# Kernel tuning notes

Measured on AMD Instinct MI355X. Metric: run time of the kernel, lower is better.

The kernel has to match this reference:

```python
import jax, jax.numpy as jnp
import numpy as np

BASE_T = 0.07
ALPHA = 0.5
EPS = 1e-12  # torch F.normalize eps


def _l2_normalize(x):
    norm = jnp.linalg.norm(x, axis=1, keepdims=True)
    return x / jnp.maximum(norm, EPS)


def setup_inputs() -> dict:
    key = jax.random.key(0)
    k1, k2, k3 = jax.random.split(key, 3)
    B, D, H, W = 4096, 512, 16, 16
    return {
        "emb1": jax.random.normal(k1, (B, D), dtype=jnp.float32),
        "emb2": jax.random.normal(k2, (B, D), dtype=jnp.float32),
        "attention_map": jax.random.uniform(k3, (B, H, W), dtype=jnp.float32),
    }


def reference(emb1, emb2, attention_map):
    B = emb1.shape[0]
    e1 = _l2_normalize(emb1)
    e2 = _l2_normalize(emb2)

    att = attention_map.mean(axis=(1, 2))                     # [B]
    temp = (BASE_T * (1.0 + ALPHA * att))[:, None]            # [B, 1]

    x = jnp.concatenate([e1, e2], axis=0)                     # [2B, D]
    x_swap = jnp.concatenate([e2, e1], axis=0)                # [2B, D]
    temp_cat = jnp.concatenate([temp, temp], axis=0)          # [2B, 1]

    sim = jnp.matmul(x, x.T) / temp_cat                       # [2B, 2B]
    pos_sim = jnp.sum(x * x_swap, axis=1) / temp_cat[:, 0]    # [2B]

    diag = jnp.eye(2 * B, dtype=bool)
    sim = jnp.where(diag, -jnp.inf, sim)                      # exp(-inf) = 0

    denominator = jnp.exp(sim).sum(axis=1)                    # [2B]
    loss = -jnp.log(jnp.exp(pos_sim) / denominator)
    return loss.mean()
```

## Files before the change

### kernel.cpp

```cpp
#include <hip/hip_runtime.h>
#include <hip/hip_bf16.h>
#include <math.h>

#define B_ROWS 4096
#define D_DIM 512
#define TWO_B 8192
#define HW_N 256
#define BASE_T 0.07f
#define ALPHA_C 0.5f
#define LOG2E 1.44269504088896340736f

typedef float v4f __attribute__((ext_vector_type(4)));

__device__ __forceinline__ float fast_exp2(float x) {
#if __has_builtin(__builtin_amdgcn_exp2f)
    return __builtin_amdgcn_exp2f(x);
#else
    return exp2f(x);
#endif
}

__global__ __launch_bounds__(256) void prep_kernel(
    const float* __restrict__ emb1, const float* __restrict__ emb2,
    const float* __restrict__ att, unsigned short* __restrict__ X8,
    float* __restrict__ inv_temp, float* __restrict__ pos)
{
    const int b = blockIdx.x;
    const int t = threadIdx.x;
    const float2 a1 = ((const float2*)(emb1 + (size_t)b * D_DIM))[t];
    const float2 a2 = ((const float2*)(emb2 + (size_t)b * D_DIM))[t];
    float av = att[(size_t)b * HW_N + t];
    float s1  = a1.x * a1.x + a1.y * a1.y;
    float s2  = a2.x * a2.x + a2.y * a2.y;
    float s12 = a1.x * a2.x + a1.y * a2.y;
    #pragma unroll
    for (int m = 1; m < 64; m <<= 1) {
        s1  += __shfl_xor(s1, m, 64);
        s2  += __shfl_xor(s2, m, 64);
        s12 += __shfl_xor(s12, m, 64);
        av  += __shfl_xor(av, m, 64);
    }
    __shared__ float red[4][4];
    const int w = t >> 6, lane = t & 63;
    if (lane == 0) { red[w][0] = s1; red[w][1] = s2; red[w][2] = s12; red[w][3] = av; }
    __syncthreads();
    const float T1  = red[0][0] + red[1][0] + red[2][0] + red[3][0];
    const float T2  = red[0][1] + red[1][1] + red[2][1] + red[3][1];
    const float T12 = red[0][2] + red[1][2] + red[2][2] + red[3][2];
    const float Ta  = red[0][3] + red[1][3] + red[2][3] + red[3][3];
    const float i1 = 1.0f / fmaxf(sqrtf(T1), 1e-12f);
    const float i2 = 1.0f / fmaxf(sqrtf(T2), 1e-12f);
    const float it = 1.0f / (BASE_T * (1.0f + ALPHA_C * (Ta * (1.0f / 256.0f))));
    const int p1 = __builtin_amdgcn_cvt_pk_fp8_f32(a1.x * i1, a1.y * i1, 0, false);
    const int p2 = __builtin_amdgcn_cvt_pk_fp8_f32(a2.x * i2, a2.y * i2, 0, false);
    X8[(size_t)b * 256 + t]            = (unsigned short)(p1 & 0xffff);
    X8[(size_t)(b + B_ROWS) * 256 + t] = (unsigned short)(p2 & 0xffff);
    if (t == 0) {
        inv_temp[b] = it * LOG2E;
        inv_temp[b + B_ROWS] = it * LOG2E;
        pos[b] = (T12 * i1 * i2) * it;
    }
}

__device__ __forceinline__ void gload_lds16(const void* g, void* s) {
    __builtin_amdgcn_global_load_lds(
        (const __attribute__((address_space(1))) unsigned int*)g,
        (__attribute__((address_space(3))) unsigned int*)s,
        16, 0, 0);
}

__global__ __launch_bounds__(256, 4) void gram_kernel(
    const unsigned char* __restrict__ X8,
    const float* __restrict__ inv_temp,
    float* __restrict__ partial)
{
    const int bid = (blockIdx.x & 7) * 260 + (blockIdx.x >> 3);
    int rb = (int)((129.0f - sqrtf(129.0f * 129.0f - 8.0f * (float)bid)) * 0.5f);
    rb = rb < 0 ? 0 : (rb > 63 ? 63 : rb);
    while (rb > 0 && (rb * (129 - rb)) / 2 > bid) rb--;
    while (rb < 63 && ((rb + 1) * (129 - (rb + 1))) / 2 <= bid) rb++;
    const int cb = rb + (bid - (rb * (129 - rb)) / 2);

    __shared__ unsigned char smA[2][8192];
    __shared__ unsigned char smB[2][8192];

    const int rowBase = rb * 128;
    const int colBase = cb * 128;

    const int tid  = threadIdx.x;
    const int w    = tid >> 6;
    const int lane = tid & 63;
    const int quad = lane >> 4;
    const int t    = lane & 15;
    const int wm   = w >> 1;
    const int wn   = w & 1;

    const int lr = lane >> 2;
    const int su = lane & 3;

    const unsigned char* Arow0 = X8 + (size_t)rowBase * D_DIM;
    const unsigned char* Brow0 = X8 + (size_t)colBase * D_DIM;

    v4f acc[4][4];
    #pragma unroll
    for (int a = 0; a < 4; a++)
        #pragma unroll
        for (int b2 = 0; b2 < 4; b2++)
            acc[a][b2] = v4f{0.0f, 0.0f, 0.0f, 0.0f};

    const int hb = (t >> 1) & 3;
    const int aBase = (wm * 64 + t) * 64;
    const int bBase = (wn * 64 + t) * 64;

    #pragma unroll
    for (int j = 0; j < 2; j++) {
        const int g = w * 2 + j;
        const int r = g * 16 + lr;
        const int gc = su ^ ((r >> 1) & 3);
        gload_lds16(Arow0 + (size_t)r * D_DIM + gc * 16, &smA[0][g * 1024]);
        gload_lds16(Brow0 + (size_t)r * D_DIM + gc * 16, &smB[0][g * 1024]);
    }
    __syncthreads();

    #pragma unroll
    for (int p = 0; p < 8; p++) {
        const int cur = p & 1;
        const int nxt = cur ^ 1;

        if (p < 7) {
            const int kk = (p + 1) * 64;
            #pragma unroll
            for (int j = 0; j < 2; j++) {
                const int g = w * 2 + j;
                const int r = g * 16 + lr;
                const int gc = su ^ ((r >> 1) & 3);
                gload_lds16(Arow0 + (size_t)r * D_DIM + kk + gc * 16, &smA[nxt][g * 1024]);
                gload_lds16(Brow0 + (size_t)r * D_DIM + kk + gc * 16, &smB[nxt][g * 1024]);
            }
        }

        #pragma unroll
        for (int s = 0; s < 2; s++) {
            const int pu = (s * 2 + (quad >> 1)) ^ hb;
            const int off = pu * 16 + (quad & 1) * 8;
            long aF[4], bF[4];
            #pragma unroll
            for (int mi = 0; mi < 4; mi++)
                aF[mi] = *(const long*)&smA[cur][aBase + mi * 1024 + off];
            #pragma unroll
            for (int ni = 0; ni < 4; ni++)
                bF[ni] = *(const long*)&smB[cur][bBase + ni * 1024 + off];
            #pragma unroll
            for (int mi = 0; mi < 4; mi++)
                #pragma unroll
                for (int ni = 0; ni < 4; ni++)
                    acc[mi][ni] = __builtin_amdgcn_mfma_f32_16x16x32_fp8_fp8(
                        aF[mi], bF[ni], acc[mi][ni], 0, 0, 0);
        }

        __syncthreads();
    }

    v4f itv[4];
    #pragma unroll
    for (int mi = 0; mi < 4; mi++)
        itv[mi] = *(const v4f*)&inv_temp[rowBase + wm * 64 + mi * 16 + quad * 4];

    float* prow = partial + (size_t)(cb * 2 + wn) * TWO_B;
    #pragma unroll
    for (int mi = 0; mi < 4; mi++) {
        #pragma unroll
        for (int r = 0; r < 4; r++) {
            const int i = rowBase + wm * 64 + mi * 16 + quad * 4 + r;
            const float it = itv[mi][r];
            float s = 0.0f;
            #pragma unroll
            for (int ni = 0; ni < 4; ni++) {
                const int j = colBase + wn * 64 + ni * 16 + t;
                const float v = fast_exp2(acc[mi][ni][r] * it);
                s += (i == j) ? 0.0f : v;
            }
            s += __shfl_xor(s, 1, 64);
            s += __shfl_xor(s, 2, 64);
            s += __shfl_xor(s, 4, 64);
            s += __shfl_xor(s, 8, 64);
            if (t == 0) prow[i] = s;
        }
    }

    if (rb != cb) {
        float itj[4];
        float cs[4] = {0.0f, 0.0f, 0.0f, 0.0f};
        #pragma unroll
        for (int ni = 0; ni < 4; ni++)
            itj[ni] = inv_temp[colBase + wn * 64 + ni * 16 + t];
        #pragma unroll
        for (int mi = 0; mi < 4; mi++)
            #pragma unroll
            for (int r = 0; r < 4; r++)
                #pragma unroll
                for (int ni = 0; ni < 4; ni++)
                    cs[ni] += fast_exp2(acc[mi][ni][r] * itj[ni]);
        float* pcol = partial + (size_t)(rb * 2 + wm) * TWO_B;
        #pragma unroll
        for (int ni = 0; ni < 4; ni++) {
            cs[ni] += __shfl_xor(cs[ni], 16, 64);
            cs[ni] += __shfl_xor(cs[ni], 32, 64);
            if (quad == 0) pcol[colBase + wn * 64 + ni * 16 + t] = cs[ni];
        }
    }
}

__global__ __launch_bounds__(256) void finish1(
    const float* __restrict__ partial, const float* __restrict__ pos,
    float* __restrict__ blockSums)
{
    const int i = blockIdx.x * 256 + threadIdx.x;
    float d = 0.0f;
    #pragma unroll 8
    for (int s = 0; s < 128; s++) d += partial[(size_t)s * TWO_B + i];
    float li = logf(d) - pos[i & (B_ROWS - 1)];
    #pragma unroll
    for (int m = 1; m < 64; m <<= 1) li += __shfl_xor(li, m, 64);
    __shared__ float red[4];
    const int w = threadIdx.x >> 6, lane = threadIdx.x & 63;
    if (lane == 0) red[w] = li;
    __syncthreads();
    if (threadIdx.x == 0) blockSums[blockIdx.x] = red[0] + red[1] + red[2] + red[3];
}

__global__ void finish2(const float* __restrict__ blockSums, float* __restrict__ out)
{
    const int lane = threadIdx.x;
    float v = (lane < 32) ? blockSums[lane] : 0.0f;
    #pragma unroll
    for (int m = 1; m < 64; m <<= 1) v += __shfl_xor(v, m, 64);
    if (lane == 0) out[0] = v * (1.0f / 8192.0f);
}

extern "C" void kernel_launch(void* const* d_in, const int* in_sizes, int n_in,
                              void* d_out, int out_size, void* d_ws, size_t ws_size,
                              hipStream_t stream) {
    const float* emb1 = (const float*)d_in[0];
    const float* emb2 = (const float*)d_in[1];
    const float* att  = (const float*)d_in[2];
    float* out = (float*)d_out;

    char* ws = (char*)d_ws;
    unsigned short* X8 = (unsigned short*)ws;
    float* inv_temp    = (float*)(ws + 4194304);
    float* pos         = (float*)(ws + 4194304 + 32768);
    float* partial     = (float*)(ws + 4194304 + 32768 + 16384);
    float* blockSums   = (float*)(ws + 4194304 + 32768 + 16384 + 4194304);

    prep_kernel<<<B_ROWS, 256, 0, stream>>>(emb1, emb2, att, X8, inv_temp, pos);
    gram_kernel<<<2080, 256, 0, stream>>>((const unsigned char*)X8, inv_temp, partial);
    finish1<<<TWO_B / 256, 256, 0, stream>>>(partial, pos, blockSums);
    finish2<<<1, 64, 0, stream>>>(blockSums, out);
}
```

Baseline: 121.3 us.

## Use 8-wave gram blocks and atomic denominator accumulation, dropping partial buffer

```diff
diff --git a/kernel.cpp b/kernel.cpp
--- a/kernel.cpp
+++ b/kernel.cpp
@@ -23,10 +23,12 @@
 __global__ __launch_bounds__(256) void prep_kernel(
     const float* __restrict__ emb1, const float* __restrict__ emb2,
     const float* __restrict__ att, unsigned short* __restrict__ X8,
-    float* __restrict__ inv_temp, float* __restrict__ pos)
+    float* __restrict__ inv_temp, float* __restrict__ pos,
+    float* __restrict__ denom, float* __restrict__ out)
 {
     const int b = blockIdx.x;
     const int t = threadIdx.x;
+    if (b < 32) denom[b * 256 + t] = 0.0f;
     const float2 a1 = ((const float2*)(emb1 + (size_t)b * D_DIM))[t];
     const float2 a2 = ((const float2*)(emb2 + (size_t)b * D_DIM))[t];
     float av = att[(size_t)b * HW_N + t];
@@ -59,6 +61,7 @@
         inv_temp[b] = it * LOG2E;
         inv_temp[b + B_ROWS] = it * LOG2E;
         pos[b] = (T12 * i1 * i2) * it;
+        if (b == 0) out[0] = 0.0f;
     }
 }
 
@@ -69,10 +72,10 @@
         16, 0, 0);
 }
 
-__global__ __launch_bounds__(256, 4) void gram_kernel(
+__global__ __launch_bounds__(512, 6) void gram_kernel(
     const unsigned char* __restrict__ X8,
     const float* __restrict__ inv_temp,
-    float* __restrict__ partial)
+    float* __restrict__ denom)
 {
     const int bid = (blockIdx.x & 7) * 260 + (blockIdx.x >> 3);
     int rb = (int)((129.0f - sqrtf(129.0f * 129.0f - 8.0f * (float)bid)) * 0.5f);
@@ -92,68 +95,59 @@
     const int lane = tid & 63;
     const int quad = lane >> 4;
     const int t    = lane & 15;
-    const int wm   = w >> 1;
-    const int wn   = w & 1;
+    const int wm   = w >> 2;
+    const int wn   = w & 3;
 
     const int lr = lane >> 2;
-    const int su = lane & 3;
+    const int su = (lane & 3) ^ ((lr >> 1) & 3);
+    const int srow = w * 16 + lr;
 
     const unsigned char* Arow0 = X8 + (size_t)rowBase * D_DIM;
     const unsigned char* Brow0 = X8 + (size_t)colBase * D_DIM;
 
-    v4f acc[4][4];
+    v4f acc[4][2];
     #pragma unroll
     for (int a = 0; a < 4; a++)
         #pragma unroll
-        for (int b2 = 0; b2 < 4; b2++)
+        for (int b2 = 0; b2 < 2; b2++)
             acc[a][b2] = v4f{0.0f, 0.0f, 0.0f, 0.0f};
 
     const int hb = (t >> 1) & 3;
     const int aBase = (wm * 64 + t) * 64;
-    const int bBase = (wn * 64 + t) * 64;
-
-    #pragma unroll
-    for (int j = 0; j < 2; j++) {
-        const int g = w * 2 + j;
-        const int r = g * 16 + lr;
-        const int gc = su ^ ((r >> 1) & 3);
-        gload_lds16(Arow0 + (size_t)r * D_DIM + gc * 16, &smA[0][g * 1024]);
-        gload_lds16(Brow0 + (size_t)r * D_DIM + gc * 16, &smB[0][g * 1024]);
+    const int bBase = (wn * 32 + t) * 64;
+
+    {
+        const size_t src = (size_t)srow * D_DIM + su * 16;
+        gload_lds16(Arow0 + src, &smA[0][w * 1024]);
+        gload_lds16(Brow0 + src, &smB[0][w * 1024]);
     }
     __syncthreads();
 
     #pragma unroll
     for (int p = 0; p < 8; p++) {
         const int cur = p & 1;
-        const int nxt = cur ^ 1;
 
         if (p < 7) {
-            const int kk = (p + 1) * 64;
-            #pragma unroll
-            for (int j = 0; j < 2; j++) {
-                const int g = w * 2 + j;
-                const int r = g * 16 + lr;
-                const int gc = su ^ ((r >> 1) & 3);
-                gload_lds16(Arow0 + (size_t)r * D_DIM + kk + gc * 16, &smA[nxt][g * 1024]);
-                gload_lds16(Brow0 + (size_t)r * D_DIM + kk + gc * 16, &smB[nxt][g * 1024]);
-            }
+            const size_t src = (size_t)srow * D_DIM + (p + 1) * 64 + su * 16;
+            gload_lds16(Arow0 + src, &smA[cur ^ 1][w * 1024]);
+            gload_lds16(Brow0 + src, &smB[cur ^ 1][w * 1024]);
         }
 
         #pragma unroll
         for (int s = 0; s < 2; s++) {
             const int pu = (s * 2 + (quad >> 1)) ^ hb;
             const int off = pu * 16 + (quad & 1) * 8;
-            long aF[4], bF[4];
+            long aF[4], bF[2];
             #pragma unroll
             for (int mi = 0; mi < 4; mi++)
                 aF[mi] = *(const long*)&smA[cur][aBase + mi * 1024 + off];
             #pragma unroll
-            for (int ni = 0; ni < 4; ni++)
+            for (int ni = 0; ni < 2; ni++)
                 bF[ni] = *(const long*)&smB[cur][bBase + ni * 1024 + off];
             #pragma unroll
             for (int mi = 0; mi < 4; mi++)
                 #pragma unroll
-                for (int ni = 0; ni < 4; ni++)
+                for (int ni = 0; ni < 2; ni++)
                     acc[mi][ni] = __builtin_amdgcn_mfma_f32_16x16x32_fp8_fp8(
                         aF[mi], bF[ni], acc[mi][ni], 0, 0, 0);
         }
@@ -166,7 +160,6 @@
     for (int mi = 0; mi < 4; mi++)
         itv[mi] = *(const v4f*)&inv_temp[rowBase + wm * 64 + mi * 16 + quad * 4];
 
-    float* prow = partial + (size_t)(cb * 2 + wn) * TWO_B;
     #pragma unroll
     for (int mi = 0; mi < 4; mi++) {
         #pragma unroll
@@ -175,8 +168,8 @@
             const float it = itv[mi][r];
             float s = 0.0f;
             #pragma unroll
-            for (int ni = 0; ni < 4; ni++) {
-                const int j = colBase + wn * 64 + ni * 16 + t;
+            for (int ni = 0; ni < 2; ni++) {
+                const int j = colBase + wn * 32 + ni * 16 + t;
                 const float v = fast_exp2(acc[mi][ni][r] * it);
                 s += (i == j) ? 0.0f : v;
             }
@@ -184,58 +177,47 @@
             s += __shfl_xor(s, 2, 64);
             s += __shfl_xor(s, 4, 64);
             s += __shfl_xor(s, 8, 64);
-            if (t == 0) prow[i] = s;
+            if (t == 0) atomicAdd(&denom[i], s);
         }
     }
 
     if (rb != cb) {
-        float itj[4];
-        float cs[4] = {0.0f, 0.0f, 0.0f, 0.0f};
-        #pragma unroll
-        for (int ni = 0; ni < 4; ni++)
-            itj[ni] = inv_temp[colBase + wn * 64 + ni * 16 + t];
+        float itj[2];
+        float cs[2] = {0.0f, 0.0f};
+        #pragma unroll
+        for (int ni = 0; ni < 2; ni++)
+            itj[ni] = inv_temp[colBase + wn * 32 + ni * 16 + t];
         #pragma unroll
         for (int mi = 0; mi < 4; mi++)
             #pragma unroll
             for (int r = 0; r < 4; r++)
                 #pragma unroll
-                for (int ni = 0; ni < 4; ni++)
+                for (int ni = 0; ni < 2; ni++)
                     cs[ni] += fast_exp2(acc[mi][ni][r] * itj[ni]);
-        float* pcol = partial + (size_t)(rb * 2 + wm) * TWO_B;
-        #pragma unroll
-        for (int ni = 0; ni < 4; ni++) {
+        #pragma unroll
+        for (int ni = 0; ni < 2; ni++) {
             cs[ni] += __shfl_xor(cs[ni], 16, 64);
             cs[ni] += __shfl_xor(cs[ni], 32, 64);
-            if (quad == 0) pcol[colBase + wn * 64 + ni * 16 + t] = cs[ni];
-        }
-    }
-}
-
-__global__ __launch_bounds__(256) void finish1(
-    const float* __restrict__ partial, const float* __restrict__ pos,
-    float* __restrict__ blockSums)
+            if (quad == 0)
+                atomicAdd(&denom[colBase + wn * 32 + ni * 16 + t], cs[ni]);
+        }
+    }
+}
+
+__global__ __launch_bounds__(256) void finishk(
+    const float* __restrict__ denom, const float* __restrict__ pos,
+    float* __restrict__ out)
 {
     const int i = blockIdx.x * 256 + threadIdx.x;
-    float d = 0.0f;
-    #pragma unroll 8
-    for (int s = 0; s < 128; s++) d += partial[(size_t)s * TWO_B + i];
-    float li = logf(d) - pos[i & (B_ROWS - 1)];
+    float li = logf(denom[i]) - pos[i & (B_ROWS - 1)];
     #pragma unroll
     for (int m = 1; m < 64; m <<= 1) li += __shfl_xor(li, m, 64);
     __shared__ float red[4];
     const int w = threadIdx.x >> 6, lane = threadIdx.x & 63;
     if (lane == 0) red[w] = li;
     __syncthreads();
-    if (threadIdx.x == 0) blockSums[blockIdx.x] = red[0] + red[1] + red[2] + red[3];
-}
-
-__global__ void finish2(const float* __restrict__ blockSums, float* __restrict__ out)
-{
-    const int lane = threadIdx.x;
-    float v = (lane < 32) ? blockSums[lane] : 0.0f;
-    #pragma unroll
-    for (int m = 1; m < 64; m <<= 1) v += __shfl_xor(v, m, 64);
-    if (lane == 0) out[0] = v * (1.0f / 8192.0f);
+    if (threadIdx.x == 0)
+        atomicAdd(out, (red[0] + red[1] + red[2] + red[3]) * (1.0f / 8192.0f));
 }
 
 extern "C" void kernel_launch(void* const* d_in, const int* in_sizes, int n_in,
@@ -250,11 +232,10 @@
     unsigned short* X8 = (unsigned short*)ws;
     float* inv_temp    = (float*)(ws + 4194304);
     float* pos         = (float*)(ws + 4194304 + 32768);
-    float* partial     = (float*)(ws + 4194304 + 32768 + 16384);
-    float* blockSums   = (float*)(ws + 4194304 + 32768 + 16384 + 4194304);
-
-    prep_kernel<<<B_ROWS, 256, 0, stream>>>(emb1, emb2, att, X8, inv_temp, pos);
-    gram_kernel<<<2080, 256, 0, stream>>>((const unsigned char*)X8, inv_temp, partial);
-    finish1<<<TWO_B / 256, 256, 0, stream>>>(partial, pos, blockSums);
-    finish2<<<1, 64, 0, stream>>>(blockSums, out);
-}
+    float* denom       = (float*)(ws + 4194304 + 32768 + 16384);
+
+    prep_kernel<<<B_ROWS, 256, 0, stream>>>(emb1, emb2, att, X8, inv_temp, pos,
+                                            denom, out);
+    gram_kernel<<<2080, 512, 0, stream>>>((const unsigned char*)X8, inv_temp, denom);
+    finishk<<<TWO_B / 256, 256, 0, stream>>>(denom, pos, out);
+}
```

Result: slower. 171.2 us (+41.2%).

## Raise gram occupancy, stagger block starts, merge final reduction via atomic

Applied to the files above, without the earlier changes.

```diff
diff --git a/kernel.cpp b/kernel.cpp
--- a/kernel.cpp
+++ b/kernel.cpp
@@ -23,7 +23,8 @@
 __global__ __launch_bounds__(256) void prep_kernel(
     const float* __restrict__ emb1, const float* __restrict__ emb2,
     const float* __restrict__ att, unsigned short* __restrict__ X8,
-    float* __restrict__ inv_temp, float* __restrict__ pos)
+    float* __restrict__ inv_temp, float* __restrict__ pos,
+    float* __restrict__ out)
 {
     const int b = blockIdx.x;
     const int t = threadIdx.x;
@@ -59,6 +60,7 @@
         inv_temp[b] = it * LOG2E;
         inv_temp[b + B_ROWS] = it * LOG2E;
         pos[b] = (T12 * i1 * i2) * it;
+        if (b == 0) out[0] = 0.0f;
     }
 }
 
@@ -69,11 +71,16 @@
         16, 0, 0);
 }
 
-__global__ __launch_bounds__(256, 4) void gram_kernel(
+__global__ __launch_bounds__(256, 5) void gram_kernel(
     const unsigned char* __restrict__ X8,
     const float* __restrict__ inv_temp,
     float* __restrict__ partial)
 {
+    {
+        const int stg = (int)((blockIdx.x >> 3) % 5u);
+        for (int z = 0; z < stg; z++) __builtin_amdgcn_s_sleep(7);
+    }
+
     const int bid = (blockIdx.x & 7) * 260 + (blockIdx.x >> 3);
     int rb = (int)((129.0f - sqrtf(129.0f * 129.0f - 8.0f * (float)bid)) * 0.5f);
     rb = rb < 0 ? 0 : (rb > 63 ? 63 : rb);
@@ -125,7 +132,6 @@
     #pragma unroll
     for (int p = 0; p < 8; p++) {
         const int cur = p & 1;
-        const int nxt = cur ^ 1;
 
         if (p < 7) {
             const int kk = (p + 1) * 64;
@@ -134,8 +140,8 @@
                 const int g = w * 2 + j;
                 const int r = g * 16 + lr;
                 const int gc = su ^ ((r >> 1) & 3);
-                gload_lds16(Arow0 + (size_t)r * D_DIM + kk + gc * 16, &smA[nxt][g * 1024]);
-                gload_lds16(Brow0 + (size_t)r * D_DIM + kk + gc * 16, &smB[nxt][g * 1024]);
+                gload_lds16(Arow0 + (size_t)r * D_DIM + kk + gc * 16, &smA[cur ^ 1][g * 1024]);
+                gload_lds16(Brow0 + (size_t)r * D_DIM + kk + gc * 16, &smB[cur ^ 1][g * 1024]);
             }
         }
 
@@ -211,9 +217,9 @@
     }
 }
 
-__global__ __launch_bounds__(256) void finish1(
+__global__ __launch_bounds__(256) void finishk(
     const float* __restrict__ partial, const float* __restrict__ pos,
-    float* __restrict__ blockSums)
+    float* __restrict__ out)
 {
     const int i = blockIdx.x * 256 + threadIdx.x;
     float d = 0.0f;
@@ -226,16 +232,8 @@
     const int w = threadIdx.x >> 6, lane = threadIdx.x & 63;
     if (lane == 0) red[w] = li;
     __syncthreads();
-    if (threadIdx.x == 0) blockSums[blockIdx.x] = red[0] + red[1] + red[2] + red[3];
-}
-
-__global__ void finish2(const float* __restrict__ blockSums, float* __restrict__ out)
-{
-    const int lane = threadIdx.x;
-    float v = (lane < 32) ? blockSums[lane] : 0.0f;
-    #pragma unroll
-    for (int m = 1; m < 64; m <<= 1) v += __shfl_xor(v, m, 64);
-    if (lane == 0) out[0] = v * (1.0f / 8192.0f);
+    if (threadIdx.x == 0)
+        atomicAdd(out, (red[0] + red[1] + red[2] + red[3]) * (1.0f / 8192.0f));
 }
 
 extern "C" void kernel_launch(void* const* d_in, const int* in_sizes, int n_in,
@@ -251,10 +249,8 @@
     float* inv_temp    = (float*)(ws + 4194304);
     float* pos         = (float*)(ws + 4194304 + 32768);
     float* partial     = (float*)(ws + 4194304 + 32768 + 16384);
-    float* blockSums   = (float*)(ws + 4194304 + 32768 + 16384 + 4194304);
-
-    prep_kernel<<<B_ROWS, 256, 0, stream>>>(emb1, emb2, att, X8, inv_temp, pos);
+
+    prep_kernel<<<B_ROWS, 256, 0, stream>>>(emb1, emb2, att, X8, inv_temp, pos, out);
     gram_kernel<<<2080, 256, 0, stream>>>((const unsigned char*)X8, inv_temp, partial);
-    finish1<<<TWO_B / 256, 256, 0, stream>>>(partial, pos, blockSums);
-    finish2<<<1, 64, 0, stream>>>(blockSums, out);
-}
+    finishk<<<TWO_B / 256, 256, 0, stream>>>(partial, pos, out);
+}
```

After: 139.7 us. 15.2% more time.
